# Kernel tuning notes

Measured on AMD Instinct MI355X. Metric: run time of the kernel, lower is better.

Reference implementation:

```python
import jax, jax.numpy as jnp
import numpy as np

E = 1024
H = 16
D = E // H  # head_dim = 64


def setup_inputs() -> dict:
    key = jax.random.key(0)
    k_x, k_w1, k_b1, k_w2, k_b2 = jax.random.split(key, 5)
    s = 1.0 / np.sqrt(E)
    return {
        "x": jax.random.normal(k_x, (2, 2048, E), dtype=jnp.float32),
        "qkv_w": jax.random.uniform(k_w1, (3 * E, E), jnp.float32, -s, s),
        "qkv_b": jax.random.uniform(k_b1, (3 * E,), jnp.float32, -s, s),
        "out_w": jax.random.uniform(k_w2, (E, E), jnp.float32, -s, s),
        "out_b": jax.random.uniform(k_b2, (E,), jnp.float32, -s, s),
    }


def reference(x, qkv_w, qkv_b, out_w, out_b):
    B, T, _ = x.shape
    # qkv projection (torch Linear: x @ W.T + b)
    qkv = x @ qkv_w.T + qkv_b  # [B, T, 3E]
    q, k, v = jnp.split(qkv, 3, axis=-1)
    # [B, T, E] -> [B, H, T, D]
    def to_heads(t):
        return t.reshape(B, T, H, D).transpose(0, 2, 1, 3)
    q, k, v = to_heads(q), to_heads(k), to_heads(v)
    scale = 1.0 / np.sqrt(D).astype(np.float32)
    scores = jnp.einsum("bhqd,bhkd->bhqk", q, k) * scale  # [B, H, T, T]
    attn = jax.nn.softmax(scores, axis=-1)
    # dropout is identity in eval mode
    out = jnp.einsum("bhqk,bhkd->bhqd", attn, v)  # [B, H, T, D]
    out = out.transpose(0, 2, 1, 3).reshape(B, T, E)
    return out @ out_w.T + out_b
```

## Files before the change

### kernel.cpp

```cpp
#include <hip/hip_runtime.h>

#define TT 2048
#define BB 2
#define EE 1024
#define HH 16
#define DD 64
#define E3 3072
#define NTOK 4096

typedef unsigned short u16;
typedef _Float16 __attribute__((ext_vector_type(8))) half8;
typedef __fp16 __attribute__((ext_vector_type(2))) fp16x2;
typedef __attribute__((ext_vector_type(4))) float f32x4;

__device__ __forceinline__ unsigned f2h(float f) {
    union { _Float16 h; u16 u; } v; v.h = (_Float16)f; return (unsigned)v.u;
}
__device__ __forceinline__ unsigned pkh(float a, float b) {
    union { fp16x2 h; unsigned u; } v;
    v.h = __builtin_amdgcn_cvt_pkrtz(a, b);
    return v.u;
}

__device__ __forceinline__ void async_ld16(const u16* g, const u16* l) {
    auto gp = reinterpret_cast<const __attribute__((address_space(1))) unsigned*>(
        reinterpret_cast<uintptr_t>(g));
    auto lp = reinterpret_cast<__attribute__((address_space(3))) unsigned*>(
        reinterpret_cast<uintptr_t>(l));
    __builtin_amdgcn_global_load_lds(gp, lp, 16, 0, 0);
}

__global__ __launch_bounds__(256) void split3(
    const float* __restrict__ x, const float* __restrict__ w1,
    const float* __restrict__ w2,
    u16* __restrict__ xh, u16* __restrict__ w1h, u16* __restrict__ w2h)
{
    const int N1 = (NTOK * EE) / 4;
    const int N2 = N1 + (E3 * EE) / 4;
    int i = blockIdx.x * 256 + threadIdx.x;
    const float* src; u16* dst; int j;
    if (i < N1)      { src = x;  dst = xh;  j = i; }
    else if (i < N2) { src = w1; dst = w1h; j = i - N1; }
    else             { src = w2; dst = w2h; j = i - N2; }
    float4 v = ((const float4*)src)[j];
    *(uint2*)&dst[(size_t)j * 4] = make_uint2(
        f2h(v.x) | (f2h(v.y) << 16), f2h(v.z) | (f2h(v.w) << 16));
}

__global__ __launch_bounds__(256) void vtrans(
    const u16* __restrict__ qkv, u16* __restrict__ vt)
{
    __shared__ u16 L[64][72];
    const int tid = threadIdx.x;
    const int t0 = blockIdx.x * 64;
    const int h  = blockIdx.y;
    const int b  = blockIdx.z;
    const int row = tid >> 2;
    const int c16 = (tid & 3) << 4;

    const u16* src = qkv + (size_t)(b * TT + t0 + row) * E3 + 2 * EE + h * DD + c16;
    *(uint4*)&L[row][c16]     = *(const uint4*)src;
    *(uint4*)&L[row][c16 + 8] = *(const uint4*)(src + 8);
    __syncthreads();

    union { uint4 u[2]; u16 s[16]; } P;
#pragma unroll
    for (int j = 0; j < 16; ++j) P.s[j] = L[c16 + j][row];
    u16* dst = vt + ((size_t)(b * HH + h) * DD + row) * TT + t0 + c16;
    *(uint4*)dst       = P.u[0];
    *(uint4*)(dst + 8) = P.u[1];
}

template <int WMT, bool QSCALE, bool F16OUT>
__global__ __launch_bounds__(256, 3) void gemm_f16(
    const u16* __restrict__ Ag, const u16* __restrict__ Wg,
    const float* __restrict__ bias, void* __restrict__ Cout, int M, int N)
{
    constexpr int BM = WMT * 32;
    constexpr int APASS = BM / 32;
    __shared__ u16 sA[BM * 64];
    __shared__ u16 sB[128 * 64];

    const int tid  = threadIdx.x;
    const int lane = tid & 63;
    const int wave = tid >> 6;
    const int quad = lane >> 4;
    const int l16  = lane & 15;
    const int wm = wave >> 1, wn = wave & 1;
    const int m0 = blockIdx.y * BM;
    const int n0 = blockIdx.x * 128;

    const int srow = tid >> 3;
    const int schk = tid & 7;

    const u16* ag[APASS]; int aldw[APASS];
#pragma unroll
    for (int p = 0; p < APASS; ++p) {
        int row = p * 32 + srow;
        ag[p] = Ag + (size_t)(m0 + row) * EE + ((schk ^ (row & 7)) << 3);
        aldw[p] = (p * 256 + wave * 64) * 8;
    }
    const u16* bg[4]; int bldw[4];
#pragma unroll
    for (int p = 0; p < 4; ++p) {
        int row = p * 32 + srow;
        bg[p] = Wg + (size_t)(n0 + row) * EE + ((schk ^ (row & 7)) << 3);
        bldw[p] = (p * 256 + wave * 64) * 8;
    }

    f32x4 acc[WMT][4];
#pragma unroll
    for (int mt = 0; mt < WMT; ++mt)
#pragma unroll
        for (int nt = 0; nt < 4; ++nt) acc[mt][nt] = (f32x4){0.f, 0.f, 0.f, 0.f};

    for (int k0 = 0; k0 < EE; k0 += 64) {
        __syncthreads();
#pragma unroll
        for (int p = 0; p < APASS; ++p) async_ld16(ag[p] + k0, sA + aldw[p]);
#pragma unroll
        for (int p = 0; p < 4; ++p)    async_ld16(bg[p] + k0, sB + bldw[p]);
        __syncthreads();

        half8 fa[WMT][2], fb[4][2];
#pragma unroll
        for (int mt = 0; mt < WMT; ++mt) {
            int r = wm * (WMT * 16) + mt * 16 + l16;
#pragma unroll
            for (int ks = 0; ks < 2; ++ks)
                fa[mt][ks] = *(const half8*)&sA[r * 64 + (((ks * 4 + quad) ^ (r & 7)) << 3)];
        }
#pragma unroll
        for (int nt = 0; nt < 4; ++nt) {
            int r = wn * 64 + nt * 16 + l16;
#pragma unroll
            for (int ks = 0; ks < 2; ++ks)
                fb[nt][ks] = *(const half8*)&sB[r * 64 + (((ks * 4 + quad) ^ (r & 7)) << 3)];
        }
#pragma unroll
        for (int ks = 0; ks < 2; ++ks)
#pragma unroll
            for (int mt = 0; mt < WMT; ++mt)
#pragma unroll
                for (int nt = 0; nt < 4; ++nt)
                    acc[mt][nt] = __builtin_amdgcn_mfma_f32_16x16x32_f16(
                        fa[mt][ks], fb[nt][ks], acc[mt][nt], 0, 0, 0);
    }

    const float scale = (QSCALE && n0 < EE) ? 0.18033688011112042f : 1.0f;
    float bv[4];
#pragma unroll
    for (int nt = 0; nt < 4; ++nt) bv[nt] = bias[n0 + wn * 64 + nt * 16 + l16];
#pragma unroll
    for (int mt = 0; mt < WMT; ++mt)
#pragma unroll
        for (int nt = 0; nt < 4; ++nt)
#pragma unroll
            for (int r = 0; r < 4; ++r) {
                int rg = m0 + wm * (WMT * 16) + mt * 16 + quad * 4 + r;
                int cg = n0 + wn * 64 + nt * 16 + l16;
                float v = (acc[mt][nt][r] + bv[nt]) * scale;
                if (F16OUT) ((u16*)Cout)[(size_t)rg * N + cg] = (u16)f2h(v);
                else        ((float*)Cout)[(size_t)rg * N + cg] = v;
            }
}

__global__ __launch_bounds__(256, 3) void attn_mfma(
    const u16* __restrict__ qkv, const u16* __restrict__ vt,
    u16* __restrict__ obuf)
{
    __shared__ u16 KB[2][64][64];
    __shared__ u16 VB[2][64][64];
    __shared__ u16 QP[128][64];

    const int tid  = threadIdx.x;
    const int wave = tid >> 6;
    const int lane = tid & 63;
    const int quad = lane >> 4;
    const int l16  = lane & 15;

    const int q0 = blockIdx.x * 128;
    const int hh = blockIdx.y;
    const int b  = blockIdx.z;

    const int srow = tid >> 3;
    const int schk = tid & 7;
    const int ldsw = wave * 512;

#pragma unroll
    for (int p = 0; p < 4; ++p) {
        int row = p * 32 + srow;
        const u16* qg = qkv + (size_t)(b * TT + q0 + row) * E3 + hh * DD
                        + ((schk ^ (row & 7)) << 3);
        async_ld16(qg, &QP[0][0] + p * 2048 + ldsw);
    }
#pragma unroll
    for (int p = 0; p < 2; ++p) {
        int row = p * 32 + srow;
        int sw8 = (schk ^ (row & 7)) << 3;
        async_ld16(qkv + (size_t)(b * TT + row) * E3 + EE + hh * DD + sw8,
                   &KB[0][0][0] + p * 2048 + ldsw);
        async_ld16(vt + ((size_t)(b * HH + hh) * DD + row) * TT + sw8,
                   &VB[0][0][0] + p * 2048 + ldsw);
    }
    __syncthreads();

    half8 qb[2][2];
#pragma unroll
    for (int qt = 0; qt < 2; ++qt) {
        int row = wave * 32 + qt * 16 + l16;
#pragma unroll
        for (int ks = 0; ks < 2; ++ks)
            qb[qt][ks] = *(const half8*)&QP[row][((ks * 4 + quad) ^ (row & 7)) << 3];
    }

    const f32x4 Z = {0.f, 0.f, 0.f, 0.f};
    float l_i[2] = {0.f, 0.f};
    f32x4 o[4][2];
#pragma unroll
    for (int dt = 0; dt < 4; ++dt)
#pragma unroll
        for (int qt = 0; qt < 2; ++qt) o[dt][qt] = (f32x4){0.f, 0.f, 0.f, 0.f};

    int cur = 0;
    for (int kt = 0; kt < TT; kt += 64, cur ^= 1) {
        const int ktn = (kt + 64) & (TT - 1);
#pragma unroll
        for (int p = 0; p < 2; ++p) {
            int row = p * 32 + srow;
            int sw8 = (schk ^ (row & 7)) << 3;
            async_ld16(qkv + (size_t)(b * TT + ktn + row) * E3 + EE + hh * DD + sw8,
                       &KB[cur ^ 1][0][0] + p * 2048 + ldsw);
            async_ld16(vt + ((size_t)(b * HH + hh) * DD + row) * TT + ktn + sw8,
                       &VB[cur ^ 1][0][0] + p * 2048 + ldsw);
        }

        f32x4 s[2][4];
#pragma unroll
        for (int nt = 0; nt < 4; ++nt) {
            int r0 = nt * 16 + l16;
            half8 kf0 = *(const half8*)&KB[cur][r0][((quad)     ^ (r0 & 7)) << 3];
            half8 kf1 = *(const half8*)&KB[cur][r0][((4 + quad) ^ (r0 & 7)) << 3];
#pragma unroll
            for (int qt = 0; qt < 2; ++qt) {
                f32x4 t = __builtin_amdgcn_mfma_f32_16x16x32_f16(kf0, qb[qt][0], Z, 0, 0, 0);
                s[qt][nt] = __builtin_amdgcn_mfma_f32_16x16x32_f16(kf1, qb[qt][1], t, 0, 0, 0);
            }
        }

#pragma unroll
        for (int qt = 0; qt < 2; ++qt) {
            int prow = wave * 32 + qt * 16 + l16;
            float rs0 = 0.f, rs1 = 0.f;
#pragma unroll
            for (int nt = 0; nt < 4; ++nt) {
                float p0 = __builtin_amdgcn_exp2f(s[qt][nt][0]);
                float p1 = __builtin_amdgcn_exp2f(s[qt][nt][1]);
                float p2 = __builtin_amdgcn_exp2f(s[qt][nt][2]);
                float p3 = __builtin_amdgcn_exp2f(s[qt][nt][3]);
                rs0 += p0 + p1;
                rs1 += p2 + p3;
                int phys = (nt * 2 + (quad >> 1)) ^ (prow & 7);
                *(uint2*)&QP[prow][phys * 8 + ((quad & 1) << 2)] =
                    make_uint2(pkh(p0, p1), pkh(p2, p3));
            }
            l_i[qt] += rs0 + rs1;
        }

#pragma unroll
        for (int ks = 0; ks < 2; ++ks) {
            half8 pf[2];
#pragma unroll
            for (int qt = 0; qt < 2; ++qt) {
                int prow = wave * 32 + qt * 16 + l16;
                pf[qt] = *(const half8*)&QP[prow][((ks * 4 + quad) ^ (prow & 7)) << 3];
            }
#pragma unroll
            for (int dt = 0; dt < 4; ++dt) {
                int vr = dt * 16 + l16;
                half8 vf = *(const half8*)&VB[cur][vr][((ks * 4 + quad) ^ (vr & 7)) << 3];
#pragma unroll
                for (int qt = 0; qt < 2; ++qt)
                    o[dt][qt] = __builtin_amdgcn_mfma_f32_16x16x32_f16(vf, pf[qt], o[dt][qt], 0, 0, 0);
            }
        }

        __syncthreads();
    }

    float inv[2];
#pragma unroll
    for (int qt = 0; qt < 2; ++qt) {
        float l = l_i[qt];
        l += __shfl_xor(l, 16, 64);
        l += __shfl_xor(l, 32, 64);
        inv[qt] = 1.f / l;
    }
#pragma unroll
    for (int qt = 0; qt < 2; ++qt) {
        size_t base = (size_t)(b * TT + q0 + wave * 32 + qt * 16 + l16) * EE + hh * DD;
#pragma unroll
        for (int dt = 0; dt < 4; ++dt) {
            unsigned hv[4];
#pragma unroll
            for (int r = 0; r < 4; ++r) hv[r] = f2h(o[dt][qt][r] * inv[qt]);
            *(uint2*)&obuf[base + dt * 16 + quad * 4] =
                make_uint2(hv[0] | (hv[1] << 16), hv[2] | (hv[3] << 16));
        }
    }
}

extern "C" void kernel_launch(void* const* d_in, const int* in_sizes, int n_in,
                              void* d_out, int out_size, void* d_ws, size_t ws_size,
                              hipStream_t stream)
{
    const float* x     = (const float*)d_in[0];
    const float* qkv_w = (const float*)d_in[1];
    const float* qkv_b = (const float*)d_in[2];
    const float* out_w = (const float*)d_in[3];
    const float* out_b = (const float*)d_in[4];
    float* out = (float*)d_out;

    const size_t NX  = (size_t)NTOK * EE;
    const size_t NW1 = (size_t)E3 * EE;
    const size_t NW2 = (size_t)EE * EE;
    const size_t NQ  = (size_t)NTOK * E3;

    u16* ws   = (u16*)d_ws;
    u16* x_h  = ws;
    u16* w1h  = ws + NX;
    u16* w2h  = w1h + NW1;
    u16* qkvb = w2h + NW2;
    u16* vtb  = qkvb + NQ;

    split3<<<dim3((unsigned)((NX + NW1 + NW2) / 4 / 256)), 256, 0, stream>>>(
        x, qkv_w, out_w, x_h, w1h, w2h);

    gemm_f16<4, true, true><<<dim3(E3 / 128, NTOK / 128), 256, 0, stream>>>(
        x_h, w1h, qkv_b, (void*)qkvb, NTOK, E3);

    vtrans<<<dim3(TT / 64, HH, BB), 256, 0, stream>>>(qkvb, vtb);

    attn_mfma<<<dim3(TT / 128, HH, BB), 256, 0, stream>>>(qkvb, vtb, x_h);

    gemm_f16<2, false, false><<<dim3(EE / 128, NTOK / 64), 256, 0, stream>>>(
        x_h, w2h, out_b, (void*)out, NTOK, EE);
}
```

Measured before the change: 193.1 us.

## Halve attention query tile to 64 rows per block for more parallelism

The attention kernel now processes 64 queries per block (16 per wave) instead of 128, doubling the grid and raising the launch-bounds occupancy hint from 3 to 4. This targets low occupancy and poor latency hiding when only a few blocks run per CU. In exchange, each K/V tile loaded into shared memory is reused by half as many queries, doubling K/V load traffic, and there is less MFMA work per wave to overlap with loads.

```diff
diff --git a/kernel.cpp b/kernel.cpp
--- a/kernel.cpp
+++ b/kernel.cpp
@@ -165,13 +165,13 @@
             }
 }
 
-__global__ __launch_bounds__(256, 3) void attn_mfma(
+__global__ __launch_bounds__(256, 4) void attn_mfma(
     const u16* __restrict__ qkv, const u16* __restrict__ vt,
     u16* __restrict__ obuf)
 {
     __shared__ u16 KB[2][64][64];
     __shared__ u16 VB[2][64][64];
-    __shared__ u16 QP[128][64];
+    __shared__ u16 QP[64][64];
 
     const int tid  = threadIdx.x;
     const int wave = tid >> 6;
@@ -179,7 +179,7 @@
     const int quad = lane >> 4;
     const int l16  = lane & 15;
 
-    const int q0 = blockIdx.x * 128;
+    const int q0 = blockIdx.x * 64;
     const int hh = blockIdx.y;
     const int b  = blockIdx.z;
 
@@ -188,7 +188,7 @@
     const int ldsw = wave * 512;
 
 #pragma unroll
-    for (int p = 0; p < 4; ++p) {
+    for (int p = 0; p < 2; ++p) {
         int row = p * 32 + srow;
         const u16* qg = qkv + (size_t)(b * TT + q0 + row) * E3 + hh * DD
                         + ((schk ^ (row & 7)) << 3);
@@ -205,22 +205,19 @@
     }
     __syncthreads();
 
-    half8 qb[2][2];
-#pragma unroll
-    for (int qt = 0; qt < 2; ++qt) {
-        int row = wave * 32 + qt * 16 + l16;
+    half8 qb[2];
+    {
+        int row = wave * 16 + l16;
 #pragma unroll
         for (int ks = 0; ks < 2; ++ks)
-            qb[qt][ks] = *(const half8*)&QP[row][((ks * 4 + quad) ^ (row & 7)) << 3];
+            qb[ks] = *(const half8*)&QP[row][((ks * 4 + quad) ^ (row & 7)) << 3];
     }
 
     const f32x4 Z = {0.f, 0.f, 0.f, 0.f};
-    float l_i[2] = {0.f, 0.f};
-    f32x4 o[4][2];
-#pragma unroll
-    for (int dt = 0; dt < 4; ++dt)
-#pragma unroll
-        for (int qt = 0; qt < 2; ++qt) o[dt][qt] = (f32x4){0.f, 0.f, 0.f, 0.f};
+    float l_i = 0.f;
+    f32x4 o[4];
+#pragma unroll
+    for (int dt = 0; dt < 4; ++dt) o[dt] = (f32x4){0.f, 0.f, 0.f, 0.f};
 
     int cur = 0;
     for (int kt = 0; kt < TT; kt += 64, cur ^= 1) {
@@ -235,75 +232,63 @@
                        &VB[cur ^ 1][0][0] + p * 2048 + ldsw);
         }
 
-        f32x4 s[2][4];
+        f32x4 s[4];
 #pragma unroll
         for (int nt = 0; nt < 4; ++nt) {
             int r0 = nt * 16 + l16;
             half8 kf0 = *(const half8*)&KB[cur][r0][((quad)     ^ (r0 & 7)) << 3];
             half8 kf1 = *(const half8*)&KB[cur][r0][((4 + quad) ^ (r0 & 7)) << 3];
-#pragma unroll
-            for (int qt = 0; qt < 2; ++qt) {
-                f32x4 t = __builtin_amdgcn_mfma_f32_16x16x32_f16(kf0, qb[qt][0], Z, 0, 0, 0);
-                s[qt][nt] = __builtin_amdgcn_mfma_f32_16x16x32_f16(kf1, qb[qt][1], t, 0, 0, 0);
-            }
-        }
-
-#pragma unroll
-        for (int qt = 0; qt < 2; ++qt) {
-            int prow = wave * 32 + qt * 16 + l16;
+            f32x4 t = __builtin_amdgcn_mfma_f32_16x16x32_f16(kf0, qb[0], Z, 0, 0, 0);
+            s[nt] = __builtin_amdgcn_mfma_f32_16x16x32_f16(kf1, qb[1], t, 0, 0, 0);
+        }
+
+        {
+            int prow = wave * 16 + l16;
             float rs0 = 0.f, rs1 = 0.f;
 #pragma unroll
             for (int nt = 0; nt < 4; ++nt) {
-                float p0 = __builtin_amdgcn_exp2f(s[qt][nt][0]);
-                float p1 = __builtin_amdgcn_exp2f(s[qt][nt][1]);
-                float p2 = __builtin_amdgcn_exp2f(s[qt][nt][2]);
-                float p3 = __builtin_amdgcn_exp2f(s[qt][nt][3]);
+                float p0 = __builtin_amdgcn_exp2f(s[nt][0]);
+                float p1 = __builtin_amdgcn_exp2f(s[nt][1]);
+                float p2 = __builtin_amdgcn_exp2f(s[nt][2]);
+                float p3 = __builtin_amdgcn_exp2f(s[nt][3]);
                 rs0 += p0 + p1;
                 rs1 += p2 + p3;
                 int phys = (nt * 2 + (quad >> 1)) ^ (prow & 7);
                 *(uint2*)&QP[prow][phys * 8 + ((quad & 1) << 2)] =
                     make_uint2(pkh(p0, p1), pkh(p2, p3));
             }
-            l_i[qt] += rs0 + rs1;
+            l_i += rs0 + rs1;
         }
 
 #pragma unroll
         for (int ks = 0; ks < 2; ++ks) {
-            half8 pf[2];
-#pragma unroll
-            for (int qt = 0; qt < 2; ++qt) {
-                int prow = wave * 32 + qt * 16 + l16;
-                pf[qt] = *(const half8*)&QP[prow][((ks * 4 + quad) ^ (prow & 7)) << 3];
-            }
+            int prow = wave * 16 + l16;
+            half8 pf = *(const half8*)&QP[prow][((ks * 4 + quad) ^ (prow & 7)) << 3];
 #pragma unroll
             for (int dt = 0; dt < 4; ++dt) {
                 int vr = dt * 16 + l16;
                 half8 vf = *(const half8*)&VB[cur][vr][((ks * 4 + quad) ^ (vr & 7)) << 3];
-#pragma unroll
-                for (int qt = 0; qt < 2; ++qt)
-                    o[dt][qt] = __builtin_amdgcn_mfma_f32_16x16x32_f16(vf, pf[qt], o[dt][qt], 0, 0, 0);
+                o[dt] = __builtin_amdgcn_mfma_f32_16x16x32_f16(vf, pf, o[dt], 0, 0, 0);
             }
         }
 
         __syncthreads();
     }
 
-    float inv[2];
-#pragma unroll
-    for (int qt = 0; qt < 2; ++qt) {
-        float l = l_i[qt];
+    float inv;
+    {
+        float l = l_i;
         l += __shfl_xor(l, 16, 64);
         l += __shfl_xor(l, 32, 64);
-        inv[qt] = 1.f / l;
-    }
-#pragma unroll
-    for (int qt = 0; qt < 2; ++qt) {
-        size_t base = (size_t)(b * TT + q0 + wave * 32 + qt * 16 + l16) * EE + hh * DD;
+        inv = 1.f / l;
+    }
+    {
+        size_t base = (size_t)(b * TT + q0 + wave * 16 + l16) * EE + hh * DD;
 #pragma unroll
         for (int dt = 0; dt < 4; ++dt) {
             unsigned hv[4];
 #pragma unroll
-            for (int r = 0; r < 4; ++r) hv[r] = f2h(o[dt][qt][r] * inv[qt]);
+            for (int r = 0; r < 4; ++r) hv[r] = f2h(o[dt][r] * inv);
             *(uint2*)&obuf[base + dt * 16 + quad * 4] =
                 make_uint2(hv[0] | (hv[1] << 16), hv[2] | (hv[3] << 16));
         }
@@ -341,7 +326,7 @@
 
     vtrans<<<dim3(TT / 64, HH, BB), 256, 0, stream>>>(qkvb, vtb);
 
-    attn_mfma<<<dim3(TT / 128, HH, BB), 256, 0, stream>>>(qkvb, vtb, x_h);
+    attn_mfma<<<dim3(TT / 64, HH, BB), 256, 0, stream>>>(qkvb, vtb, x_h);
 
     gemm_f16<2, false, false><<<dim3(EE / 128, NTOK / 64), 256, 0, stream>>>(
         x_h, w2h, out_b, (void*)out, NTOK, EE);
```

After: 190.5 us. Within noise of the previous version (-1.4%).

## Keep softmax probabilities in registers and feed PV MFMA directly

Applied to the files above, without the earlier changes.

The attention kernel no longer round-trips the probability tile through shared memory. It uses the 16x16x16 MFMA, whose B operand layout matches the S accumulator layout, so exp2'd scores are packed to fp16 and fed straight into the PV product per 16-key group. Q fragments are loaded directly from global memory into registers, and the block shrinks to 128 threads covering 64 queries, doubling the grid. This trades the LDS traffic and the extra barrier for twice as many smaller MFMA instructions and more K/V tile loads per query.

```diff
diff --git a/kernel.cpp b/kernel.cpp
--- a/kernel.cpp
+++ b/kernel.cpp
@@ -10,16 +10,15 @@
 
 typedef unsigned short u16;
 typedef _Float16 __attribute__((ext_vector_type(8))) half8;
+typedef _Float16 __attribute__((ext_vector_type(4))) half4;
 typedef __fp16 __attribute__((ext_vector_type(2))) fp16x2;
 typedef __attribute__((ext_vector_type(4))) float f32x4;
 
 __device__ __forceinline__ unsigned f2h(float f) {
     union { _Float16 h; u16 u; } v; v.h = (_Float16)f; return (unsigned)v.u;
 }
-__device__ __forceinline__ unsigned pkh(float a, float b) {
-    union { fp16x2 h; unsigned u; } v;
-    v.h = __builtin_amdgcn_cvt_pkrtz(a, b);
-    return v.u;
+__device__ __forceinline__ fp16x2 pk2(float a, float b) {
+    return __builtin_amdgcn_cvt_pkrtz(a, b);
 }
 
 __device__ __forceinline__ void async_ld16(const u16* g, const u16* l) {
@@ -165,13 +164,12 @@
             }
 }
 
-__global__ __launch_bounds__(256, 3) void attn_mfma(
+__global__ __launch_bounds__(128, 2) void attn_mfma(
     const u16* __restrict__ qkv, const u16* __restrict__ vt,
     u16* __restrict__ obuf)
 {
     __shared__ u16 KB[2][64][64];
     __shared__ u16 VB[2][64][64];
-    __shared__ u16 QP[128][64];
 
     const int tid  = threadIdx.x;
     const int wave = tid >> 6;
@@ -179,7 +177,7 @@
     const int quad = lane >> 4;
     const int l16  = lane & 15;
 
-    const int q0 = blockIdx.x * 128;
+    const int q0 = blockIdx.x * 64;
     const int hh = blockIdx.y;
     const int b  = blockIdx.z;
 
@@ -187,32 +185,26 @@
     const int schk = tid & 7;
     const int ldsw = wave * 512;
 
+    half8 qb[2][2];
+#pragma unroll
+    for (int qt = 0; qt < 2; ++qt) {
+        int row = q0 + wave * 32 + qt * 16 + l16;
+        const u16* qg = qkv + (size_t)(b * TT + row) * E3 + hh * DD;
+#pragma unroll
+        for (int ks = 0; ks < 2; ++ks)
+            qb[qt][ks] = *(const half8*)(qg + ks * 32 + quad * 8);
+    }
+
 #pragma unroll
     for (int p = 0; p < 4; ++p) {
-        int row = p * 32 + srow;
-        const u16* qg = qkv + (size_t)(b * TT + q0 + row) * E3 + hh * DD
-                        + ((schk ^ (row & 7)) << 3);
-        async_ld16(qg, &QP[0][0] + p * 2048 + ldsw);
-    }
-#pragma unroll
-    for (int p = 0; p < 2; ++p) {
-        int row = p * 32 + srow;
+        int row = p * 16 + srow;
         int sw8 = (schk ^ (row & 7)) << 3;
         async_ld16(qkv + (size_t)(b * TT + row) * E3 + EE + hh * DD + sw8,
-                   &KB[0][0][0] + p * 2048 + ldsw);
+                   &KB[0][0][0] + p * 1024 + ldsw);
         async_ld16(vt + ((size_t)(b * HH + hh) * DD + row) * TT + sw8,
-                   &VB[0][0][0] + p * 2048 + ldsw);
+                   &VB[0][0][0] + p * 1024 + ldsw);
     }
     __syncthreads();
-
-    half8 qb[2][2];
-#pragma unroll
-    for (int qt = 0; qt < 2; ++qt) {
-        int row = wave * 32 + qt * 16 + l16;
-#pragma unroll
-        for (int ks = 0; ks < 2; ++ks)
-            qb[qt][ks] = *(const half8*)&QP[row][((ks * 4 + quad) ^ (row & 7)) << 3];
-    }
 
     const f32x4 Z = {0.f, 0.f, 0.f, 0.f};
     float l_i[2] = {0.f, 0.f};
@@ -226,62 +218,43 @@
     for (int kt = 0; kt < TT; kt += 64, cur ^= 1) {
         const int ktn = (kt + 64) & (TT - 1);
 #pragma unroll
-        for (int p = 0; p < 2; ++p) {
-            int row = p * 32 + srow;
+        for (int p = 0; p < 4; ++p) {
+            int row = p * 16 + srow;
             int sw8 = (schk ^ (row & 7)) << 3;
             async_ld16(qkv + (size_t)(b * TT + ktn + row) * E3 + EE + hh * DD + sw8,
-                       &KB[cur ^ 1][0][0] + p * 2048 + ldsw);
+                       &KB[cur ^ 1][0][0] + p * 1024 + ldsw);
             async_ld16(vt + ((size_t)(b * HH + hh) * DD + row) * TT + ktn + sw8,
-                       &VB[cur ^ 1][0][0] + p * 2048 + ldsw);
-        }
-
-        f32x4 s[2][4];
-#pragma unroll
-        for (int nt = 0; nt < 4; ++nt) {
-            int r0 = nt * 16 + l16;
+                       &VB[cur ^ 1][0][0] + p * 1024 + ldsw);
+        }
+
+#pragma unroll
+        for (int kg = 0; kg < 4; ++kg) {
+            int r0 = kg * 16 + l16;
             half8 kf0 = *(const half8*)&KB[cur][r0][((quad)     ^ (r0 & 7)) << 3];
             half8 kf1 = *(const half8*)&KB[cur][r0][((4 + quad) ^ (r0 & 7)) << 3];
+
+            half4 pb[2];
 #pragma unroll
             for (int qt = 0; qt < 2; ++qt) {
                 f32x4 t = __builtin_amdgcn_mfma_f32_16x16x32_f16(kf0, qb[qt][0], Z, 0, 0, 0);
-                s[qt][nt] = __builtin_amdgcn_mfma_f32_16x16x32_f16(kf1, qb[qt][1], t, 0, 0, 0);
-            }
-        }
-
-#pragma unroll
-        for (int qt = 0; qt < 2; ++qt) {
-            int prow = wave * 32 + qt * 16 + l16;
-            float rs0 = 0.f, rs1 = 0.f;
-#pragma unroll
-            for (int nt = 0; nt < 4; ++nt) {
-                float p0 = __builtin_amdgcn_exp2f(s[qt][nt][0]);
-                float p1 = __builtin_amdgcn_exp2f(s[qt][nt][1]);
-                float p2 = __builtin_amdgcn_exp2f(s[qt][nt][2]);
-                float p3 = __builtin_amdgcn_exp2f(s[qt][nt][3]);
-                rs0 += p0 + p1;
-                rs1 += p2 + p3;
-                int phys = (nt * 2 + (quad >> 1)) ^ (prow & 7);
-                *(uint2*)&QP[prow][phys * 8 + ((quad & 1) << 2)] =
-                    make_uint2(pkh(p0, p1), pkh(p2, p3));
-            }
-            l_i[qt] += rs0 + rs1;
-        }
-
-#pragma unroll
-        for (int ks = 0; ks < 2; ++ks) {
-            half8 pf[2];
-#pragma unroll
-            for (int qt = 0; qt < 2; ++qt) {
-                int prow = wave * 32 + qt * 16 + l16;
-                pf[qt] = *(const half8*)&QP[prow][((ks * 4 + quad) ^ (prow & 7)) << 3];
+                f32x4 s = __builtin_amdgcn_mfma_f32_16x16x32_f16(kf1, qb[qt][1], t, 0, 0, 0);
+                float p0 = __builtin_amdgcn_exp2f(s[0]);
+                float p1 = __builtin_amdgcn_exp2f(s[1]);
+                float p2 = __builtin_amdgcn_exp2f(s[2]);
+                float p3 = __builtin_amdgcn_exp2f(s[3]);
+                l_i[qt] += (p0 + p1) + (p2 + p3);
+                union { fp16x2 h[2]; half4 v; } u;
+                u.h[0] = pk2(p0, p1);
+                u.h[1] = pk2(p2, p3);
+                pb[qt] = u.v;
             }
 #pragma unroll
             for (int dt = 0; dt < 4; ++dt) {
                 int vr = dt * 16 + l16;
-                half8 vf = *(const half8*)&VB[cur][vr][((ks * 4 + quad) ^ (vr & 7)) << 3];
-#pragma unroll
-                for (int qt = 0; qt < 2; ++qt)
-                    o[dt][qt] = __builtin_amdgcn_mfma_f32_16x16x32_f16(vf, pf[qt], o[dt][qt], 0, 0, 0);
+                int chunk = (kg * 2 + (quad >> 1)) ^ (vr & 7);
+                half4 vf = *(const half4*)&VB[cur][vr][chunk * 8 + ((quad & 1) << 2)];
+                o[dt][0] = __builtin_amdgcn_mfma_f32_16x16x16f16(vf, pb[0], o[dt][0], 0, 0, 0);
+                o[dt][1] = __builtin_amdgcn_mfma_f32_16x16x16f16(vf, pb[1], o[dt][1], 0, 0, 0);
             }
         }
 
@@ -341,7 +314,7 @@
 
     vtrans<<<dim3(TT / 64, HH, BB), 256, 0, stream>>>(qkvb, vtb);
 
-    attn_mfma<<<dim3(TT / 128, HH, BB), 256, 0, stream>>>(qkvb, vtb, x_h);
+    attn_mfma<<<dim3(TT / 64, HH, BB), 128, 0, stream>>>(qkvb, vtb, x_h);
 
     gemm_f16<2, false, false><<<dim3(EE / 128, NTOK / 64), 256, 0, stream>>>(
         x_h, w2h, out_b, (void*)out, NTOK, EE);
```

After: 188.2 us. 2.6% less time.
